# Kernel optimization log

Measured on AMD Instinct MI355X. Metric: run time of the kernel, lower is better.

The kernel has to match this reference:

```python
import jax, jax.numpy as jnp
import numpy as np

DIM = 1024
B, SQ, SK = 8, 2048, 2048


def setup_inputs() -> dict:
    key = jax.random.key(0)
    ks = jax.random.split(key, 8)
    s = 1.0 / np.sqrt(DIM)
    return {
        "x": jax.random.normal(ks[0], (B, SQ, DIM), dtype=jnp.float32),
        "context": jax.random.normal(ks[1], (B, SK, DIM), dtype=jnp.float32),
        "Wq": jax.random.normal(ks[2], (DIM, DIM), dtype=jnp.float32) * s,
        "bq": jnp.zeros((DIM,), dtype=jnp.float32),
        "Wk": jax.random.normal(ks[3], (DIM, DIM), dtype=jnp.float32) * s,
        "bk": jnp.zeros((DIM,), dtype=jnp.float32),
        "Wv": jax.random.normal(ks[4], (DIM, DIM), dtype=jnp.float32) * s,
        "bv": jnp.zeros((DIM,), dtype=jnp.float32),
    }


def reference(x, context, Wq, bq, Wk, bk, Wv, bv):
    # nn.Linear: y = x @ W.T + b
    q = jnp.einsum("bsd,ed->bse", x, Wq) + bq          # [B, SQ, D]
    k = jnp.einsum("btd,ed->bte", context, Wk) + bk    # [B, SK, D]
    v = jnp.einsum("btd,ed->bte", context, Wv) + bv    # [B, SK, D]
    scale = 1.0 / jnp.sqrt(jnp.asarray(x.shape[-1], dtype=x.dtype))
    scores = jnp.einsum("bse,bte->bst", q, k) * scale  # [B, SQ, SK]
    attn = jax.nn.softmax(scores, axis=-1)
    return jnp.einsum("bst,bte->bse", attn, v)         # [B, SQ, D]
```

## Files before the change

kernel.cpp:

```cpp
#include <hip/hip_runtime.h>
#include <hip/hip_bf16.h>
#include <hip/hip_fp16.h>

typedef float f32x4 __attribute__((ext_vector_type(4)));
typedef short short8 __attribute__((ext_vector_type(8)));
typedef _Float16 h4 __attribute__((ext_vector_type(4)));
typedef unsigned short u16;
typedef unsigned int u32;

#define BK 32

__device__ __forceinline__ u16 bf16_rne(float x) {
  u32 u = __float_as_uint(x);
  u += 0x7FFFu + ((u >> 16) & 1u);
  return (u16)(u >> 16);
}
__device__ __forceinline__ u32 pack2(float a, float b) {
  return (u32)bf16_rne(a) | ((u32)bf16_rne(b) << 16);
}

__global__ __launch_bounds__(256)
void convert_kernel(const float* __restrict__ x, const float* __restrict__ ctx,
                    const float* __restrict__ wq, const float* __restrict__ wk,
                    const float* __restrict__ wv,
                    u16* __restrict__ xb, u16* __restrict__ cb,
                    u16* __restrict__ wqb, u16* __restrict__ wkb,
                    u16* __restrict__ wvb)
{
  int blk = blockIdx.x;
  const float* src; u16* dst; size_t off;
  if (blk < 8192)       { src = x;   dst = xb;  off = (size_t)blk * 2048; }
  else if (blk < 16384) { src = ctx; dst = cb;  off = (size_t)(blk - 8192) * 2048; }
  else if (blk < 16896) { src = wq;  dst = wqb; off = (size_t)(blk - 16384) * 2048; }
  else if (blk < 17408) { src = wk;  dst = wkb; off = (size_t)(blk - 16896) * 2048; }
  else                  { src = wv;  dst = wvb; off = (size_t)(blk - 17408) * 2048; }
  size_t e = off + (size_t)threadIdx.x * 8;
  float4 a = *(const float4*)(src + e);
  float4 b = *(const float4*)(src + e + 4);
  uint4 o;
  o.x = pack2(a.x, a.y); o.y = pack2(a.z, a.w);
  o.z = pack2(b.x, b.y); o.w = pack2(b.z, b.w);
  *(uint4*)(dst + e) = o;
}

__device__ __forceinline__ void stage_async(const u16* __restrict__ G, int ld,
                                            u16* L, int w, int lane)
{
  const int r_in = lane >> 2;
  const int scol = ((lane & 3) ^ ((r_in >> 1) & 3)) * 8;
#pragma unroll
  for (int it = 0; it < 2; ++it) {
    const int rbase = w * 32 + it * 16;
    const u16* g = G + (size_t)(rbase + r_in) * ld + scol;
    u16* l = L + rbase * BK;
    __builtin_amdgcn_global_load_lds(
        (const __attribute__((address_space(1))) void*)g,
        (__attribute__((address_space(3))) void*)l, 16, 0, 0);
  }
}

#define GEMM_FRAGS_AND_MFMA(Ah, Bh)                                            \
  short8 a_f[4], b_f[4];                                                       \
  _Pragma("unroll")                                                            \
  for (int i = 0; i < 4; ++i) {                                                \
    a_f[i] = *(const short8*)&Ah[(wm + i * 16 + lrow) * BK + sq8];             \
    b_f[i] = *(const short8*)&Bh[(wn + i * 16 + lrow) * BK + sq8];             \
  }                                                                            \
  _Pragma("unroll")                                                            \
  for (int i = 0; i < 4; ++i)                                                  \
    _Pragma("unroll")                                                          \
    for (int j = 0; j < 4; ++j)                                                \
      acc[i][j] = __builtin_amdgcn_mfma_f32_16x16x32_bf16(a_f[i], b_f[j], acc[i][j], 0, 0, 0);

#define GEMM_PROLOGUE                                                          \
  const int tid = threadIdx.x;                                                 \
  const int w = tid >> 6, lane = tid & 63;                                     \
  const int wm = (w >> 1) * 64, wn = (w & 1) * 64;                             \
  const int lrow = lane & 15, quad = lane >> 4;                                \
  const int sq8 = (quad ^ ((lrow >> 1) & 3)) * 8;                              \
  f32x4 acc[4][4];                                                             \
  _Pragma("unroll")                                                            \
  for (int i = 0; i < 4; ++i)                                                  \
    _Pragma("unroll")                                                          \
    for (int j = 0; j < 4; ++j) {                                              \
      f32x4 z = {0.f, 0.f, 0.f, 0.f};                                          \
      acc[i][j] = z;                                                           \
    }

__global__ __launch_bounds__(256)
void projq_kernel(const u16* __restrict__ A, const u16* __restrict__ W,
                  const float* __restrict__ bias, u16* __restrict__ Y)
{
  __shared__ __align__(16) u16 Ah[128 * BK];
  __shared__ __align__(16) u16 Bh[128 * BK];
  const int m0 = blockIdx.y * 128, n0 = blockIdx.x * 128;
  GEMM_PROLOGUE
  const u16* A_b = A + (size_t)m0 * 1024;
  const u16* B_b = W + (size_t)n0 * 1024;

  for (int kt = 0; kt < 1024; kt += 32) {
    __syncthreads();
    stage_async(A_b + kt, 1024, Ah, w, lane);
    stage_async(B_b + kt, 1024, Bh, w, lane);
    __syncthreads();
    GEMM_FRAGS_AND_MFMA(Ah, Bh)
  }

#pragma unroll
  for (int j = 0; j < 4; ++j) {
    int gn = n0 + wn + j * 16 + lrow;
    float bj = bias[gn];
#pragma unroll
    for (int i = 0; i < 4; ++i) {
      int gm_base = m0 + wm + i * 16 + quad * 4;
#pragma unroll
      for (int r = 0; r < 4; ++r)
        Y[(size_t)(gm_base + r) * 1024 + gn] = bf16_rne(acc[i][j][r] + bj);
    }
  }
}

__global__ __launch_bounds__(256)
void projv_kernel(const u16* __restrict__ A, const u16* __restrict__ W,
                  const float* __restrict__ bias, u16* __restrict__ Vt)
{
  __shared__ __align__(16) u16 smem[128 * 136];
  u16* Ah = smem;
  u16* Bh = smem + 128 * BK;
  const int m0 = blockIdx.y * 128, n0 = blockIdx.x * 128;
  const int bb = m0 >> 11, t0 = m0 & 2047;
  GEMM_PROLOGUE
  const u16* A_b = A + (size_t)m0 * 1024;
  const u16* B_b = W + (size_t)n0 * 1024;

  for (int kt = 0; kt < 1024; kt += 32) {
    __syncthreads();
    stage_async(A_b + kt, 1024, Ah, w, lane);
    stage_async(B_b + kt, 1024, Bh, w, lane);
    __syncthreads();
    GEMM_FRAGS_AND_MFMA(Ah, Bh)
  }

  __syncthreads();
  u16* T = smem;
#pragma unroll
  for (int j = 0; j < 4; ++j) {
    int e_l = wn + j * 16 + lrow;
    float bj = bias[n0 + e_l];
#pragma unroll
    for (int i = 0; i < 4; ++i) {
      int t_l = wm + i * 16 + quad * 4;
      uint2 p;
      p.x = pack2(acc[i][j][0] + bj, acc[i][j][1] + bj);
      p.y = pack2(acc[i][j][2] + bj, acc[i][j][3] + bj);
      *(uint2*)&T[e_l * 136 + t_l] = p;
    }
  }
  __syncthreads();

  int e_l = tid >> 1, half = tid & 1;
  u16* gdst = Vt + ((size_t)(bb * 1024 + n0 + e_l)) * 2048 + t0 + half * 64;
  const u16* Trow = &T[e_l * 136 + half * 64];
#pragma unroll
  for (int k = 0; k < 8; ++k)
    *(uint4*)(gdst + k * 8) = *(const uint4*)(Trow + k * 8);
}

__global__ __launch_bounds__(256)
void score_kernel(const u16* __restrict__ qb, const u16* __restrict__ kb,
                  _Float16* __restrict__ S)
{
  __shared__ __align__(16) u16 Ah[128 * BK];
  __shared__ __align__(16) u16 Bh[128 * BK];
  const int b = blockIdx.z;
  const int m0 = blockIdx.y * 128, n0 = blockIdx.x * 128;
  GEMM_PROLOGUE
  const u16* A_b = qb + ((size_t)b * 2048 + m0) * 1024;
  const u16* B_b = kb + ((size_t)b * 2048 + n0) * 1024;

  for (int kt = 0; kt < 1024; kt += 32) {
    __syncthreads();
    stage_async(A_b + kt, 1024, Ah, w, lane);
    stage_async(B_b + kt, 1024, Bh, w, lane);
    __syncthreads();
    GEMM_FRAGS_AND_MFMA(Ah, Bh)
  }

  const float scale = 0.03125f;
#pragma unroll
  for (int j = 0; j < 4; ++j) {
    int gn = n0 + wn + j * 16 + lrow;
#pragma unroll
    for (int i = 0; i < 4; ++i) {
      int gm_base = m0 + wm + i * 16 + quad * 4;
#pragma unroll
      for (int r = 0; r < 4; ++r)
        S[((size_t)b * 2048 + gm_base + r) * 2048 + gn] = (_Float16)(acc[i][j][r] * scale);
    }
  }
}

__global__ __launch_bounds__(256)
void softmax_kernel(_Float16* __restrict__ S)
{
  const int row = blockIdx.x;
  const int tid = threadIdx.x;
  _Float16* Sr = S + (size_t)row * 2048;
  h4 ah = *(const h4*)(Sr + tid * 4);
  h4 bh = *(const h4*)(Sr + 1024 + tid * 4);
  float a0 = (float)ah.x, a1 = (float)ah.y, a2 = (float)ah.z, a3 = (float)ah.w;
  float b0 = (float)bh.x, b1 = (float)bh.y, b2 = (float)bh.z, b3 = (float)bh.w;

  float m = fmaxf(fmaxf(fmaxf(a0, a1), fmaxf(a2, a3)),
                  fmaxf(fmaxf(b0, b1), fmaxf(b2, b3)));
#pragma unroll
  for (int off = 32; off > 0; off >>= 1) m = fmaxf(m, __shfl_xor(m, off));

  __shared__ float red[4];
  const int wid = tid >> 6, lane = tid & 63;
  if (lane == 0) red[wid] = m;
  __syncthreads();
  m = fmaxf(fmaxf(red[0], red[1]), fmaxf(red[2], red[3]));

  float e0 = __expf(a0 - m), e1 = __expf(a1 - m), e2 = __expf(a2 - m), e3 = __expf(a3 - m);
  float e4 = __expf(b0 - m), e5 = __expf(b1 - m), e6 = __expf(b2 - m), e7 = __expf(b3 - m);
  float s = ((e0 + e1) + (e2 + e3)) + ((e4 + e5) + (e6 + e7));
#pragma unroll
  for (int off = 32; off > 0; off >>= 1) s += __shfl_xor(s, off);
  __syncthreads();
  if (lane == 0) red[wid] = s;
  __syncthreads();
  s = red[0] + red[1] + red[2] + red[3];
  float inv = 1.0f / s;

  u16* P = (u16*)S;
  size_t pb = (size_t)row * 2048;
  uint2 w0, w1;
  w0.x = pack2(e0 * inv, e1 * inv);
  w0.y = pack2(e2 * inv, e3 * inv);
  w1.x = pack2(e4 * inv, e5 * inv);
  w1.y = pack2(e6 * inv, e7 * inv);
  *(uint2*)&P[pb + tid * 4] = w0;
  *(uint2*)&P[pb + 1024 + tid * 4] = w1;
}

__global__ __launch_bounds__(256)
void pv_kernel(const u16* __restrict__ P, const u16* __restrict__ Vt,
               float* __restrict__ O)
{
  __shared__ __align__(16) u16 Ah[128 * BK];
  __shared__ __align__(16) u16 Bh[128 * BK];
  const int b = blockIdx.z;
  const int m0 = blockIdx.y * 128, n0 = blockIdx.x * 128;
  GEMM_PROLOGUE
  const u16* A_b = P + ((size_t)b * 2048 + m0) * 2048;
  const u16* B_b = Vt + ((size_t)b * 1024 + n0) * 2048;

  for (int kt = 0; kt < 2048; kt += 32) {
    __syncthreads();
    stage_async(A_b + kt, 2048, Ah, w, lane);
    stage_async(B_b + kt, 2048, Bh, w, lane);
    __syncthreads();
    GEMM_FRAGS_AND_MFMA(Ah, Bh)
  }

#pragma unroll
  for (int j = 0; j < 4; ++j) {
    int gn = n0 + wn + j * 16 + lrow;
#pragma unroll
    for (int i = 0; i < 4; ++i) {
      int gm_base = m0 + wm + i * 16 + quad * 4;
#pragma unroll
      for (int r = 0; r < 4; ++r)
        O[((size_t)b * 2048 + gm_base + r) * 1024 + gn] = acc[i][j][r];
    }
  }
}

extern "C" void kernel_launch(void* const* d_in, const int* in_sizes, int n_in,
                              void* d_out, int out_size, void* d_ws, size_t ws_size,
                              hipStream_t stream) {
  const float* x   = (const float*)d_in[0];
  const float* ctx = (const float*)d_in[1];
  const float* Wq  = (const float*)d_in[2];
  const float* bq  = (const float*)d_in[3];
  const float* Wk  = (const float*)d_in[4];
  const float* bk  = (const float*)d_in[5];
  const float* Wv  = (const float*)d_in[6];
  const float* bv  = (const float*)d_in[7];
  float* out = (float*)d_out;

  const size_t NQ = (size_t)16384 * 1024;
  const size_t NW = (size_t)1024 * 1024;
  const size_t needed = (5 * NQ + 3 * NW) * sizeof(u16);
  if (ws_size < needed) return;

  u16* xb  = (u16*)d_ws;
  u16* cb  = xb + NQ;
  u16* qb  = cb + NQ;
  u16* kb  = qb + NQ;
  u16* vt  = kb + NQ;
  u16* wqb = vt + NQ;
  u16* wkb = wqb + NW;
  u16* wvb = wkb + NW;
  _Float16* S = (_Float16*)d_ws;

  dim3 blk(256, 1, 1);
  hipLaunchKernelGGL(convert_kernel, dim3(17920, 1, 1), blk, 0, stream,
                     x, ctx, Wq, Wk, Wv, xb, cb, wqb, wkb, wvb);
  hipLaunchKernelGGL(projq_kernel, dim3(8, 128, 1), blk, 0, stream, xb, wqb, bq, qb);
  hipLaunchKernelGGL(projq_kernel, dim3(8, 128, 1), blk, 0, stream, cb, wkb, bk, kb);
  hipLaunchKernelGGL(projv_kernel, dim3(8, 128, 1), blk, 0, stream, cb, wvb, bv, vt);
  hipLaunchKernelGGL(score_kernel, dim3(16, 16, 8), blk, 0, stream, qb, kb, S);
  hipLaunchKernelGGL(softmax_kernel, dim3(16384, 1, 1), blk, 0, stream, S);
  hipLaunchKernelGGL(pv_kernel, dim3(8, 16, 8), blk, 0, stream, (const u16*)S, vt, out);
}
```

Before: 559.2 us.

## Rewrite GEMMs as 256x256 tiles with double-buffered LDS pipeline

All four GEMM stages (Q/K/V projections, scores, PV) now share one templated 256x256-tile, 512-thread main loop. It uses a 64-wide k step and a ping-pong LDS buffer of 128 KB, with XOR-swizzled async global-to-LDS loads. The loads are interleaved with quarter-block MFMA groups and managed through explicit vmcnt/lgkmcnt waits, raw barriers and s_setprio. This replaces the single-buffered 128x128, BK=32 loop, aiming to hide load latency and improve operand reuse per LDS byte. In exchange, occupancy drops to one large block per CU, grid counts shrink, and the hand-written wait counts are easy to get wrong.

Result: faster. 514.5 us (-8.0%).

```diff
diff --git a/kernel.cpp b/kernel.cpp
--- a/kernel.cpp
+++ b/kernel.cpp
@@ -7,8 +7,6 @@
 typedef _Float16 h4 __attribute__((ext_vector_type(4)));
 typedef unsigned short u16;
 typedef unsigned int u32;
-
-#define BK 32
 
 __device__ __forceinline__ u16 bf16_rne(float x) {
   u32 u = __float_as_uint(x);
@@ -43,159 +41,232 @@
   *(uint4*)(dst + e) = o;
 }
 
-__device__ __forceinline__ void stage_async(const u16* __restrict__ G, int ld,
-                                            u16* L, int w, int lane)
-{
-  const int r_in = lane >> 2;
-  const int scol = ((lane & 3) ^ ((r_in >> 1) & 3)) * 8;
+#define BARRIER() __builtin_amdgcn_s_barrier()
+#define LGKM0() do { asm volatile("s_waitcnt lgkmcnt(0)" ::: "memory"); \
+                     __builtin_amdgcn_sched_barrier(0); } while (0)
+#define VMCNT(n) asm volatile("s_waitcnt vmcnt(" #n ")" ::: "memory")
+
+__device__ __forceinline__ void stage_half(const u16* __restrict__ Gt, int ld2,
+                                           char* dst, int w, int lane)
+{
+  const int rsub = lane >> 3;
+  const int cbx = ((lane & 7) * 16) ^ (((lane >> 5) & 1) << 5);
 #pragma unroll
   for (int it = 0; it < 2; ++it) {
-    const int rbase = w * 32 + it * 16;
-    const u16* g = G + (size_t)(rbase + r_in) * ld + scol;
-    u16* l = L + rbase * BK;
+    const char* g = (const char*)Gt + (size_t)(it * 64 + w * 8 + rsub) * ld2 + cbx;
+    char* l = dst + it * 8192 + w * 1024;
     __builtin_amdgcn_global_load_lds(
         (const __attribute__((address_space(1))) void*)g,
         (__attribute__((address_space(3))) void*)l, 16, 0, 0);
   }
 }
 
-#define GEMM_FRAGS_AND_MFMA(Ah, Bh)                                            \
-  short8 a_f[4], b_f[4];                                                       \
+#define MFMA_BLK(i0, j0, AF)                                                   \
   _Pragma("unroll")                                                            \
-  for (int i = 0; i < 4; ++i) {                                                \
-    a_f[i] = *(const short8*)&Ah[(wm + i * 16 + lrow) * BK + sq8];             \
-    b_f[i] = *(const short8*)&Bh[(wn + i * 16 + lrow) * BK + sq8];             \
-  }                                                                            \
-  _Pragma("unroll")                                                            \
-  for (int i = 0; i < 4; ++i)                                                  \
+  for (int ii = 0; ii < 4; ++ii)                                               \
     _Pragma("unroll")                                                          \
-    for (int j = 0; j < 4; ++j)                                                \
-      acc[i][j] = __builtin_amdgcn_mfma_f32_16x16x32_bf16(a_f[i], b_f[j], acc[i][j], 0, 0, 0);
-
-#define GEMM_PROLOGUE                                                          \
+    for (int jj = 0; jj < 2; ++jj)                                             \
+      _Pragma("unroll")                                                        \
+      for (int kk = 0; kk < 2; ++kk)                                           \
+        acc[(i0) + ii][(j0) + jj] = __builtin_amdgcn_mfma_f32_16x16x32_bf16(   \
+            AF[ii * 2 + kk], bb[jj * 2 + kk], acc[(i0) + ii][(j0) + jj], 0, 0, 0);
+
+template <int NT, int LDA, int LDB>
+__device__ __forceinline__ void gemm256(const u16* __restrict__ A_b,
+                                        const u16* __restrict__ B_b,
+                                        char* sm, f32x4 (&acc)[8][4])
+{
+  const int tid = threadIdx.x;
+  const int w = tid >> 6, lane = tid & 63;
+  const int wr = w >> 2, wc = w & 3;
+  const int lrow = lane & 15, quad = lane >> 4;
+  const int sx = ((lrow >> 2) & 1) << 5;
+  const int cb0 = (quad * 16) ^ sx;
+  const int cb1 = (64 + quad * 16) ^ sx;
+  char* aRd = sm + wr * 16384;
+  char* bRd = sm + 32768 + (wc >> 1) * 16384;
+  const int bR0 = (wc & 1) * 64;
+
+  short8 aL[8], aH[8], bb[4];
+
+#define ST_A(p, h, t) stage_half(A_b + (size_t)((h) * 128) * LDA + (t) * 64,   \
+                                 LDA * 2, sm + (p) * 65536 + (h) * 16384, w, lane)
+#define ST_B(p, h, t) stage_half(B_b + (size_t)((h) * 128) * LDB + (t) * 64,   \
+                                 LDB * 2, sm + (p) * 65536 + 32768 + (h) * 16384, w, lane)
+#define RD8(base, R, cb) (*(const short8*)((base) + (R) * 128 + (cb)))
+
+  ST_A(0, 0, 0); ST_A(0, 1, 0); ST_B(0, 0, 0); ST_B(0, 1, 0);
+  ST_A(1, 0, 1); ST_A(1, 1, 1);
+  VMCNT(4);
+  BARRIER();
+
+  for (int t0 = 0; t0 < NT; t0 += 2) {
+    const int t1 = t0 + 1;
+    const int t2 = (t0 + 2 < NT) ? t0 + 2 : NT - 1;
+    const int t3 = (t0 + 3 < NT) ? t0 + 3 : NT - 1;
+#pragma unroll
+    for (int p = 0; p < 2; ++p) {
+      const char* aP = aRd + p * 65536;
+      const char* bP = bRd + p * 65536;
+      const int tB = p ? t2 : t1;
+      const int tA = p ? t3 : t2;
+#pragma unroll
+      for (int i = 0; i < 4; ++i) {
+        const int R = i * 16 + lrow;
+        aL[i * 2]     = RD8(aP, R, cb0);
+        aL[i * 2 + 1] = RD8(aP, R, cb1);
+      }
+#pragma unroll
+      for (int j = 0; j < 2; ++j) {
+        const int R = bR0 + j * 16 + lrow;
+        bb[j * 2]     = RD8(bP, R, cb0);
+        bb[j * 2 + 1] = RD8(bP, R, cb1);
+      }
+      ST_B(p ^ 1, 0, tB);
+      BARRIER(); LGKM0();
+      __builtin_amdgcn_s_setprio(1);
+      MFMA_BLK(0, 0, aL);
+      __builtin_amdgcn_s_setprio(0);
+      BARRIER();
+#pragma unroll
+      for (int i = 0; i < 4; ++i) {
+        const int R = 64 + i * 16 + lrow;
+        aH[i * 2]     = RD8(aP, R, cb0);
+        aH[i * 2 + 1] = RD8(aP, R, cb1);
+      }
+      ST_B(p ^ 1, 1, tB);
+      BARRIER(); LGKM0();
+      __builtin_amdgcn_s_setprio(1);
+      MFMA_BLK(4, 0, aH);
+      __builtin_amdgcn_s_setprio(0);
+      BARRIER();
+#pragma unroll
+      for (int j = 0; j < 2; ++j) {
+        const int R = bR0 + 32 + j * 16 + lrow;
+        bb[j * 2]     = RD8(bP, R, cb0);
+        bb[j * 2 + 1] = RD8(bP, R, cb1);
+      }
+      ST_A(p, 0, tA);
+      BARRIER(); LGKM0();
+      __builtin_amdgcn_s_setprio(1);
+      MFMA_BLK(0, 2, aL);
+      __builtin_amdgcn_s_setprio(0);
+      BARRIER();
+      ST_A(p, 1, tA);
+      BARRIER();
+      __builtin_amdgcn_s_setprio(1);
+      MFMA_BLK(4, 2, aH);
+      __builtin_amdgcn_s_setprio(0);
+      VMCNT(4);
+      BARRIER();
+    }
+  }
+#undef ST_A
+#undef ST_B
+#undef RD8
+}
+
+#define ACC_INIT                                                               \
+  f32x4 acc[8][4];                                                             \
+  _Pragma("unroll") for (int i = 0; i < 8; ++i)                                \
+  _Pragma("unroll") for (int j = 0; j < 4; ++j) {                              \
+    f32x4 z = {0.f, 0.f, 0.f, 0.f}; acc[i][j] = z; }
+
+#define EPI_IDX                                                                \
   const int tid = threadIdx.x;                                                 \
   const int w = tid >> 6, lane = tid & 63;                                     \
-  const int wm = (w >> 1) * 64, wn = (w & 1) * 64;                             \
+  const int wr = w >> 2, wc = w & 3;                                           \
   const int lrow = lane & 15, quad = lane >> 4;                                \
-  const int sq8 = (quad ^ ((lrow >> 1) & 3)) * 8;                              \
-  f32x4 acc[4][4];                                                             \
-  _Pragma("unroll")                                                            \
-  for (int i = 0; i < 4; ++i)                                                  \
-    _Pragma("unroll")                                                          \
-    for (int j = 0; j < 4; ++j) {                                              \
-      f32x4 z = {0.f, 0.f, 0.f, 0.f};                                          \
-      acc[i][j] = z;                                                           \
-    }
-
-__global__ __launch_bounds__(256)
-void projq_kernel(const u16* __restrict__ A, const u16* __restrict__ W,
-                  const float* __restrict__ bias, u16* __restrict__ Y)
-{
-  __shared__ __align__(16) u16 Ah[128 * BK];
-  __shared__ __align__(16) u16 Bh[128 * BK];
-  const int m0 = blockIdx.y * 128, n0 = blockIdx.x * 128;
-  GEMM_PROLOGUE
-  const u16* A_b = A + (size_t)m0 * 1024;
-  const u16* B_b = W + (size_t)n0 * 1024;
-
-  for (int kt = 0; kt < 1024; kt += 32) {
+  (void)w;
+
+__global__ __launch_bounds__(512, 2)
+void projq256_kernel(const u16* __restrict__ A, const u16* __restrict__ W,
+                     const float* __restrict__ bias, u16* __restrict__ Y)
+{
+  __shared__ __align__(16) char sm[131072];
+  const int m0 = blockIdx.y * 256, n0 = blockIdx.x * 256;
+  ACC_INIT;
+  gemm256<16, 1024, 1024>(A + (size_t)m0 * 1024, W + (size_t)n0 * 1024, sm, acc);
+  EPI_IDX;
+#pragma unroll
+  for (int j = 0; j < 4; ++j) {
+    const int gn = n0 + wc * 64 + j * 16 + lrow;
+    const float bj = bias[gn];
+#pragma unroll
+    for (int i = 0; i < 8; ++i) {
+      const int gm = m0 + wr * 128 + i * 16 + quad * 4;
+#pragma unroll
+      for (int r = 0; r < 4; ++r)
+        Y[(size_t)(gm + r) * 1024 + gn] = bf16_rne(acc[i][j][r] + bj);
+    }
+  }
+}
+
+__global__ __launch_bounds__(512, 2)
+void projv256_kernel(const u16* __restrict__ A, const u16* __restrict__ W,
+                     const float* __restrict__ bias, u16* __restrict__ Vt)
+{
+  __shared__ __align__(16) char sm[131072];
+  const int m0 = blockIdx.y * 256, n0 = blockIdx.x * 256;
+  const int bblk = m0 >> 11, t0g = m0 & 2047;
+  ACC_INIT;
+  gemm256<16, 1024, 1024>(A + (size_t)m0 * 1024, W + (size_t)n0 * 1024, sm, acc);
+  EPI_IDX;
+  VMCNT(0); BARRIER();
+
+  u16* T = (u16*)sm;
+#pragma unroll
+  for (int ch = 0; ch < 2; ++ch) {
+    BARRIER();
+    if ((wc >> 1) == ch) {
+#pragma unroll
+      for (int j = 0; j < 4; ++j) {
+        const int e_loc = (wc & 1) * 64 + j * 16 + lrow;
+        const float bj = bias[n0 + ch * 128 + e_loc];
+#pragma unroll
+        for (int i = 0; i < 8; ++i) {
+          const int t_l = wr * 128 + i * 16 + quad * 4;
+          uint2 pk;
+          pk.x = pack2(acc[i][j][0] + bj, acc[i][j][1] + bj);
+          pk.y = pack2(acc[i][j][2] + bj, acc[i][j][3] + bj);
+          *(uint2*)&T[e_loc * 264 + t_l] = pk;
+        }
+      }
+    }
     __syncthreads();
-    stage_async(A_b + kt, 1024, Ah, w, lane);
-    stage_async(B_b + kt, 1024, Bh, w, lane);
+    {
+      const int row = tid >> 2, part = tid & 3;
+      u16* gd = Vt + ((size_t)(bblk * 1024 + n0 + ch * 128 + row)) * 2048 + t0g + part * 64;
+      const u16* Tr = &T[row * 264 + part * 64];
+#pragma unroll
+      for (int k = 0; k < 8; ++k)
+        *(uint4*)(gd + k * 8) = *(const uint4*)(Tr + k * 8);
+    }
     __syncthreads();
-    GEMM_FRAGS_AND_MFMA(Ah, Bh)
-  }
-
+  }
+}
+
+__global__ __launch_bounds__(512, 2)
+void score256_kernel(const u16* __restrict__ qb, const u16* __restrict__ kb,
+                     _Float16* __restrict__ S)
+{
+  __shared__ __align__(16) char sm[131072];
+  const int b = blockIdx.z;
+  const int m0 = blockIdx.y * 256, n0 = blockIdx.x * 256;
+  ACC_INIT;
+  gemm256<16, 1024, 1024>(qb + ((size_t)b * 2048 + m0) * 1024,
+                          kb + ((size_t)b * 2048 + n0) * 1024, sm, acc);
+  EPI_IDX;
+  const float scale = 0.03125f;
 #pragma unroll
   for (int j = 0; j < 4; ++j) {
-    int gn = n0 + wn + j * 16 + lrow;
-    float bj = bias[gn];
-#pragma unroll
-    for (int i = 0; i < 4; ++i) {
-      int gm_base = m0 + wm + i * 16 + quad * 4;
+    const int gn = n0 + wc * 64 + j * 16 + lrow;
+#pragma unroll
+    for (int i = 0; i < 8; ++i) {
+      const int gm = m0 + wr * 128 + i * 16 + quad * 4;
 #pragma unroll
       for (int r = 0; r < 4; ++r)
-        Y[(size_t)(gm_base + r) * 1024 + gn] = bf16_rne(acc[i][j][r] + bj);
-    }
-  }
-}
-
-__global__ __launch_bounds__(256)
-void projv_kernel(const u16* __restrict__ A, const u16* __restrict__ W,
-                  const float* __restrict__ bias, u16* __restrict__ Vt)
-{
-  __shared__ __align__(16) u16 smem[128 * 136];
-  u16* Ah = smem;
-  u16* Bh = smem + 128 * BK;
-  const int m0 = blockIdx.y * 128, n0 = blockIdx.x * 128;
-  const int bb = m0 >> 11, t0 = m0 & 2047;
-  GEMM_PROLOGUE
-  const u16* A_b = A + (size_t)m0 * 1024;
-  const u16* B_b = W + (size_t)n0 * 1024;
-
-  for (int kt = 0; kt < 1024; kt += 32) {
-    __syncthreads();
-    stage_async(A_b + kt, 1024, Ah, w, lane);
-    stage_async(B_b + kt, 1024, Bh, w, lane);
-    __syncthreads();
-    GEMM_FRAGS_AND_MFMA(Ah, Bh)
-  }
-
-  __syncthreads();
-  u16* T = smem;
-#pragma unroll
-  for (int j = 0; j < 4; ++j) {
-    int e_l = wn + j * 16 + lrow;
-    float bj = bias[n0 + e_l];
-#pragma unroll
-    for (int i = 0; i < 4; ++i) {
-      int t_l = wm + i * 16 + quad * 4;
-      uint2 p;
-      p.x = pack2(acc[i][j][0] + bj, acc[i][j][1] + bj);
-      p.y = pack2(acc[i][j][2] + bj, acc[i][j][3] + bj);
-      *(uint2*)&T[e_l * 136 + t_l] = p;
-    }
-  }
-  __syncthreads();
-
-  int e_l = tid >> 1, half = tid & 1;
-  u16* gdst = Vt + ((size_t)(bb * 1024 + n0 + e_l)) * 2048 + t0 + half * 64;
-  const u16* Trow = &T[e_l * 136 + half * 64];
-#pragma unroll
-  for (int k = 0; k < 8; ++k)
-    *(uint4*)(gdst + k * 8) = *(const uint4*)(Trow + k * 8);
-}
-
-__global__ __launch_bounds__(256)
-void score_kernel(const u16* __restrict__ qb, const u16* __restrict__ kb,
-                  _Float16* __restrict__ S)
-{
-  __shared__ __align__(16) u16 Ah[128 * BK];
-  __shared__ __align__(16) u16 Bh[128 * BK];
-  const int b = blockIdx.z;
-  const int m0 = blockIdx.y * 128, n0 = blockIdx.x * 128;
-  GEMM_PROLOGUE
-  const u16* A_b = qb + ((size_t)b * 2048 + m0) * 1024;
-  const u16* B_b = kb + ((size_t)b * 2048 + n0) * 1024;
-
-  for (int kt = 0; kt < 1024; kt += 32) {
-    __syncthreads();
-    stage_async(A_b + kt, 1024, Ah, w, lane);
-    stage_async(B_b + kt, 1024, Bh, w, lane);
-    __syncthreads();
-    GEMM_FRAGS_AND_MFMA(Ah, Bh)
-  }
-
-  const float scale = 0.03125f;
-#pragma unroll
-  for (int j = 0; j < 4; ++j) {
-    int gn = n0 + wn + j * 16 + lrow;
-#pragma unroll
-    for (int i = 0; i < 4; ++i) {
-      int gm_base = m0 + wm + i * 16 + quad * 4;
-#pragma unroll
-      for (int r = 0; r < 4; ++r)
-        S[((size_t)b * 2048 + gm_base + r) * 2048 + gn] = (_Float16)(acc[i][j][r] * scale);
+        S[((size_t)b * 2048 + gm + r) * 2048 + gn] = (_Float16)(acc[i][j][r] * scale);
     }
   }
 }
@@ -244,35 +315,26 @@
   *(uint2*)&P[pb + 1024 + tid * 4] = w1;
 }
 
-__global__ __launch_bounds__(256)
-void pv_kernel(const u16* __restrict__ P, const u16* __restrict__ Vt,
-               float* __restrict__ O)
-{
-  __shared__ __align__(16) u16 Ah[128 * BK];
-  __shared__ __align__(16) u16 Bh[128 * BK];
+__global__ __launch_bounds__(512, 2)
+void pv256_kernel(const u16* __restrict__ P, const u16* __restrict__ Vt,
+                  float* __restrict__ O)
+{
+  __shared__ __align__(16) char sm[131072];
   const int b = blockIdx.z;
-  const int m0 = blockIdx.y * 128, n0 = blockIdx.x * 128;
-  GEMM_PROLOGUE
-  const u16* A_b = P + ((size_t)b * 2048 + m0) * 2048;
-  const u16* B_b = Vt + ((size_t)b * 1024 + n0) * 2048;
-
-  for (int kt = 0; kt < 2048; kt += 32) {
-    __syncthreads();
-    stage_async(A_b + kt, 2048, Ah, w, lane);
-    stage_async(B_b + kt, 2048, Bh, w, lane);
-    __syncthreads();
-    GEMM_FRAGS_AND_MFMA(Ah, Bh)
-  }
-
+  const int m0 = blockIdx.y * 256, n0 = blockIdx.x * 256;
+  ACC_INIT;
+  gemm256<32, 2048, 2048>(P + ((size_t)b * 2048 + m0) * 2048,
+                          Vt + ((size_t)b * 1024 + n0) * 2048, sm, acc);
+  EPI_IDX;
 #pragma unroll
   for (int j = 0; j < 4; ++j) {
-    int gn = n0 + wn + j * 16 + lrow;
-#pragma unroll
-    for (int i = 0; i < 4; ++i) {
-      int gm_base = m0 + wm + i * 16 + quad * 4;
+    const int gn = n0 + wc * 64 + j * 16 + lrow;
+#pragma unroll
+    for (int i = 0; i < 8; ++i) {
+      const int gm = m0 + wr * 128 + i * 16 + quad * 4;
 #pragma unroll
       for (int r = 0; r < 4; ++r)
-        O[((size_t)b * 2048 + gm_base + r) * 1024 + gn] = acc[i][j][r];
+        O[((size_t)b * 2048 + gm + r) * 1024 + gn] = acc[i][j][r];
     }
   }
 }
@@ -305,13 +367,14 @@
   u16* wvb = wkb + NW;
   _Float16* S = (_Float16*)d_ws;
 
-  dim3 blk(256, 1, 1);
-  hipLaunchKernelGGL(convert_kernel, dim3(17920, 1, 1), blk, 0, stream,
+  dim3 blk256(256, 1, 1);
+  dim3 blk512(512, 1, 1);
+  hipLaunchKernelGGL(convert_kernel, dim3(17920, 1, 1), blk256, 0, stream,
                      x, ctx, Wq, Wk, Wv, xb, cb, wqb, wkb, wvb);
-  hipLaunchKernelGGL(projq_kernel, dim3(8, 128, 1), blk, 0, stream, xb, wqb, bq, qb);
-  hipLaunchKernelGGL(projq_kernel, dim3(8, 128, 1), blk, 0, stream, cb, wkb, bk, kb);
-  hipLaunchKernelGGL(projv_kernel, dim3(8, 128, 1), blk, 0, stream, cb, wvb, bv, vt);
-  hipLaunchKernelGGL(score_kernel, dim3(16, 16, 8), blk, 0, stream, qb, kb, S);
-  hipLaunchKernelGGL(softmax_kernel, dim3(16384, 1, 1), blk, 0, stream, S);
-  hipLaunchKernelGGL(pv_kernel, dim3(8, 16, 8), blk, 0, stream, (const u16*)S, vt, out);
-}
+  hipLaunchKernelGGL(projq256_kernel, dim3(4, 64, 1), blk512, 0, stream, xb, wqb, bq, qb);
+  hipLaunchKernelGGL(projq256_kernel, dim3(4, 64, 1), blk512, 0, stream, cb, wkb, bk, kb);
+  hipLaunchKernelGGL(projv256_kernel, dim3(4, 64, 1), blk512, 0, stream, cb, wvb, bv, vt);
+  hipLaunchKernelGGL(score256_kernel, dim3(8, 8, 8), blk512, 0, stream, qb, kb, S);
+  hipLaunchKernelGGL(softmax_kernel, dim3(16384, 1, 1), blk256, 0, stream, S);
+  hipLaunchKernelGGL(pv256_kernel, dim3(4, 8, 8), blk512, 0, stream, (const u16*)S, vt, out);
+}
```
